# Kernel optimization log

Hardware: AMD Instinct MI355X
Metric: run time of the kernel (lower is better)

Reference implementation:

```python
import jax, jax.numpy as jnp
import numpy as np

N = 100000
E = 1600000
D_IN, D_HID, D_OUT = 128, 512, 256
EPS1 = 1e-9
BN_EPS = 1e-5


def setup_inputs() -> dict:
    key = jax.random.key(0)
    ks = jax.random.split(key, 8)
    return {
        "x": jax.random.normal(ks[0], (N, D_IN), dtype=jnp.float32),
        "edge_src": jax.random.randint(ks[1], (E,), 0, N, dtype=jnp.int32),
        "edge_dst": jax.random.randint(ks[2], (E,), 0, N, dtype=jnp.int32),
        "edge_weight": jax.random.uniform(ks[3], (E,), dtype=jnp.float32),
        "w1": jax.random.normal(ks[4], (D_IN, D_HID), dtype=jnp.float32) * (1.0 / np.sqrt(D_IN)),
        "b1": jnp.zeros((D_HID,), dtype=jnp.float32),
        "gamma": jnp.ones((D_HID,), dtype=jnp.float32),
        "beta": jnp.zeros((D_HID,), dtype=jnp.float32),
        "w2": jax.random.normal(ks[5], (D_HID, D_OUT), dtype=jnp.float32) * (1.0 / np.sqrt(D_HID)),
        "b2": jnp.zeros((D_OUT,), dtype=jnp.float32),
    }


def reference(x, edge_src, edge_dst, edge_weight, w1, b1, gamma, beta, w2, b2):
    # spmm(adj, x): gather source features, scale by edge weight, scatter-add to dst
    agg = jax.ops.segment_sum(x[edge_src] * edge_weight[:, None], edge_dst,
                              num_segments=x.shape[0])  # [N, D_IN]
    h = (1.0 + EPS1) * x + agg
    # mlp1: Linear -> BatchNorm1d (training-mode batch stats) -> ReLU -> Linear
    h = h @ w1 + b1  # [N, D_HID]
    mean = jnp.mean(h, axis=0)
    var = jnp.var(h, axis=0)  # biased variance, matching torch BN normalization
    h = (h - mean) * jax.lax.rsqrt(var + BN_EPS) * gamma + beta
    h = jax.nn.relu(h)
    return h @ w2 + b2  # [N, D_OUT]
```

## Files before the change

kernel.cpp:

```cpp
#include <hip/hip_runtime.h>
#include <hip/hip_bf16.h>

#define N_NODES 100000
#define N_EDGES 1600000
#define D_IN    128
#define D_HID   512
#define D_OUT   256

typedef __attribute__((ext_vector_type(8))) short bf16x8;
typedef __attribute__((ext_vector_type(4))) float f32x4;
typedef __attribute__((ext_vector_type(8))) unsigned short ushort8;

__device__ __forceinline__ short f2bf(float f) {
  union { float f; unsigned u; } un; un.f = f;
  unsigned r = un.u + 0x7fffu + ((un.u >> 16) & 1u);
  return (short)(r >> 16);
}
__device__ __forceinline__ float bf2f(unsigned short s) {
  union { unsigned u; float f; } un; un.u = ((unsigned)s) << 16; return un.f;
}
__device__ __forceinline__ void load_lds16(const void* g, void* l) {
  __builtin_amdgcn_global_load_lds(
      (const __attribute__((address_space(1))) char*)g,
      (__attribute__((address_space(3))) char*)l, 16, 0, 0);
}

__global__ __launch_bounds__(256) void k_prep(const float* __restrict__ w1,
                                              const float* __restrict__ w2,
                                              short* __restrict__ w1t,
                                              short* __restrict__ w2t,
                                              float* __restrict__ s1,
                                              float* __restrict__ s2,
                                              int* __restrict__ deg) {
  int gid = blockIdx.x * 256 + threadIdx.x;
  if (gid < D_IN * D_HID) {
    int n = gid >> 7, k = gid & 127;
    w1t[gid] = f2bf(w1[k * D_HID + n]);
  }
  int g2 = gid - D_IN * D_HID;
  if (g2 >= 0 && g2 < D_HID * D_OUT) {
    int n = g2 >> 9, k = g2 & 511;
    w2t[g2] = f2bf(w2[k * D_OUT + n]);
  }
  if (gid < D_HID) { s1[gid] = 0.f; s2[gid] = 0.f; }
  if (gid < N_NODES) deg[gid] = 0;
}

__global__ __launch_bounds__(256) void k_hist(const int* __restrict__ edst,
                                              int* __restrict__ deg) {
  int e = blockIdx.x * 256 + threadIdx.x;
  if (e < N_EDGES) atomicAdd(&deg[edst[e]], 1);
}

__global__ __launch_bounds__(1024) void k_scan(const int* __restrict__ deg,
                                               int* __restrict__ rowptr,
                                               int* __restrict__ cursor) {
  __shared__ int wsum[16];
  __shared__ int carry_s;
  int t = threadIdx.x;
  int lane = t & 63, w = t >> 6;
  if (t == 0) carry_s = 0;
  __syncthreads();
  for (int base = 0; base < N_NODES; base += 1024) {
    int i = base + t;
    int v = (i < N_NODES) ? deg[i] : 0;
    int sv = v;
    #pragma unroll
    for (int off = 1; off < 64; off <<= 1) {
      int u = __shfl_up(sv, off);
      if (lane >= off) sv += u;
    }
    if (lane == 63) wsum[w] = sv;
    __syncthreads();
    if (t < 16) {
      int ws = wsum[t];
      int ss = ws;
      #pragma unroll
      for (int off = 1; off < 16; off <<= 1) {
        int u = __shfl_up(ss, off);
        if (t >= off) ss += u;
      }
      wsum[t] = ss - ws;
    }
    __syncthreads();
    int incl = sv + wsum[w];
    int carry = carry_s;
    if (i < N_NODES) {
      int excl = carry + incl - v;
      rowptr[i] = excl;
      cursor[i] = excl;
    }
    __syncthreads();
    if (t == 1023) carry_s = carry + incl;
    __syncthreads();
  }
  if (t == 0) rowptr[N_NODES] = carry_s;
}

__global__ __launch_bounds__(256) void k_fill(const int* __restrict__ esrc,
                                              const int* __restrict__ edst,
                                              const float* __restrict__ ew,
                                              int* __restrict__ cursor,
                                              int2* __restrict__ recs) {
  int e = blockIdx.x * 256 + threadIdx.x;
  if (e < N_EDGES) {
    int d = edst[e];
    int slot = atomicAdd(&cursor[d], 1);
    int2 r;
    r.x = esrc[e];
    r.y = __float_as_int(ew[e]);
    recs[slot] = r;
  }
}

__global__ __launch_bounds__(256) void k_agg(const float* __restrict__ x,
                                             const int* __restrict__ rowptr,
                                             const int2* __restrict__ recs,
                                             unsigned short* __restrict__ aggb) {
  int gw = (blockIdx.x * 256 + threadIdx.x) >> 6;
  int lane = threadIdx.x & 63;
  if (gw >= N_NODES) return;
  int start = rowptr[gw], end = rowptr[gw + 1];
  float2 acc = *reinterpret_cast<const float2*>(x + (size_t)gw * D_IN + lane * 2);
  const float s0 = 1.0f + 1e-9f;
  acc.x *= s0; acc.y *= s0;
  for (int j = start; j < end; j += 64) {
    int cnt = end - j;
    if (cnt > 64) cnt = 64;
    int src = 0; float wt = 0.f;
    if (lane < cnt) {
      int2 r = recs[j + lane];
      src = r.x;
      wt = __int_as_float(r.y);
    }
    for (int jj = 0; jj < cnt; ++jj) {
      int s = __shfl(src, jj);
      float ww = __shfl(wt, jj);
      float2 xv = *reinterpret_cast<const float2*>(x + (size_t)s * D_IN + lane * 2);
      acc.x += ww * xv.x;
      acc.y += ww * xv.y;
    }
  }
  ushort2 o;
  o.x = (unsigned short)f2bf(acc.x);
  o.y = (unsigned short)f2bf(acc.y);
  *reinterpret_cast<ushort2*>(aggb + (size_t)gw * D_IN + lane * 2) = o;
}

__global__ __launch_bounds__(256) void k_gemm1(const unsigned short* __restrict__ aggb,
                                               const short* __restrict__ w1t,
                                               const float* __restrict__ b1,
                                               short* __restrict__ h1,
                                               float* __restrict__ s1,
                                               float* __restrict__ s2, int M) {
  __shared__ short As[128 * 64];
  __shared__ short Bs[128 * 64];
  int t = threadIdx.x;
  int bid = blockIdx.x;
  int nt = bid & 3, mt = bid >> 2;
  int wid = t >> 6, lane = t & 63;
  int wr = wid >> 1, wc = wid & 1;
  f32x4 acc[4][4] = {};

  for (int kt = 0; kt < 2; ++kt) {
    #pragma unroll
    for (int i = 0; i < 4; ++i) {
      int c = wid * 4 + i;
      int row = c * 8 + (lane >> 3);
      const unsigned short* g = aggb + (size_t)(mt * 128 + row) * D_IN + kt * 64 + (lane & 7) * 8;
      load_lds16(g, As + c * 512);
    }
    #pragma unroll
    for (int i = 0; i < 4; ++i) {
      int c = wid * 4 + i;
      int row = c * 8 + (lane >> 3);
      const short* g = w1t + (size_t)(nt * 128 + row) * D_IN + kt * 64 + (lane & 7) * 8;
      load_lds16(g, Bs + c * 512);
    }
    __syncthreads();
    #pragma unroll
    for (int kk = 0; kk < 2; ++kk) {
      bf16x8 af[4], bfr[4];
      #pragma unroll
      for (int mf = 0; mf < 4; ++mf)
        af[mf] = *reinterpret_cast<const bf16x8*>(As + (wr * 64 + mf * 16 + (lane & 15)) * 64 + kk * 32 + (lane >> 4) * 8);
      #pragma unroll
      for (int nf = 0; nf < 4; ++nf)
        bfr[nf] = *reinterpret_cast<const bf16x8*>(Bs + (wc * 64 + nf * 16 + (lane & 15)) * 64 + kk * 32 + (lane >> 4) * 8);
      #pragma unroll
      for (int mf = 0; mf < 4; ++mf)
        #pragma unroll
        for (int nf = 0; nf < 4; ++nf)
          acc[mf][nf] = __builtin_amdgcn_mfma_f32_16x16x32_bf16(af[mf], bfr[nf], acc[mf][nf], 0, 0, 0);
    }
    __syncthreads();
  }

  int colbase = nt * 128 + wc * 64;
  float ps[4] = {0, 0, 0, 0}, ps2[4] = {0, 0, 0, 0};
  #pragma unroll
  for (int mf = 0; mf < 4; ++mf)
    #pragma unroll
    for (int nf = 0; nf < 4; ++nf) {
      int col = colbase + nf * 16 + (lane & 15);
      float bb = b1[col];
      #pragma unroll
      for (int r = 0; r < 4; ++r) {
        int grow = mt * 128 + wr * 64 + mf * 16 + (lane >> 4) * 4 + r;
        if (grow < M) {
          float v = acc[mf][nf][r] + bb;
          h1[(size_t)grow * D_HID + col] = f2bf(v);
          ps[nf] += v; ps2[nf] += v * v;
        }
      }
    }
  #pragma unroll
  for (int nf = 0; nf < 4; ++nf) {
    float a = ps[nf], b = ps2[nf];
    a += __shfl_xor(a, 16); a += __shfl_xor(a, 32);
    b += __shfl_xor(b, 16); b += __shfl_xor(b, 32);
    if ((lane >> 4) == 0) {
      int col = colbase + nf * 16 + lane;
      unsafeAtomicAdd(&s1[col], a);
      unsafeAtomicAdd(&s2[col], b);
    }
  }
}

__global__ void k_bn(const float* __restrict__ s1, const float* __restrict__ s2,
                     const float* __restrict__ gamma, const float* __restrict__ beta,
                     float* __restrict__ A, float* __restrict__ C) {
  int i = threadIdx.x;
  float inv_n = 1.0f / (float)N_NODES;
  float mean = s1[i] * inv_n;
  float var = s2[i] * inv_n - mean * mean;
  float a = gamma[i] * rsqrtf(var + 1e-5f);
  A[i] = a;
  C[i] = beta[i] - mean * a;
}

__global__ __launch_bounds__(256) void k_gemm2(const unsigned short* __restrict__ h1,
                                               const short* __restrict__ w2t,
                                               const float* __restrict__ b2,
                                               const float* __restrict__ Abn,
                                               const float* __restrict__ Cbn,
                                               float* __restrict__ out, int M) {
  __shared__ short As[128 * 64];
  __shared__ short Bs[128 * 64];
  __shared__ float aL[D_HID], cL[D_HID];
  int t = threadIdx.x;
  for (int i = t; i < D_HID; i += 256) { aL[i] = Abn[i]; cL[i] = Cbn[i]; }
  __syncthreads();

  int bid = blockIdx.x;
  int nt = bid & 1, mt = bid >> 1;
  int wid = t >> 6, lane = t & 63;
  int wr = wid >> 1, wc = wid & 1;
  f32x4 acc[4][4] = {};

  for (int kt = 0; kt < 8; ++kt) {
    #pragma unroll
    for (int i = 0; i < 4; ++i) {
      int idx = i * 2048 + t * 8;
      int row = idx >> 6, k = idx & 63;
      int grow = mt * 128 + row;
      ushort8 res = {};
      if (grow < M) {
        ushort8 u = *reinterpret_cast<const ushort8*>(h1 + (size_t)grow * D_HID + kt * 64 + k);
        #pragma unroll
        for (int j = 0; j < 8; ++j) {
          int gk = kt * 64 + k + j;
          float v = bf2f(u[j]) * aL[gk] + cL[gk];
          v = fmaxf(v, 0.f);
          res[j] = (unsigned short)f2bf(v);
        }
      }
      *reinterpret_cast<ushort8*>(As + idx) = res;
    }
    #pragma unroll
    for (int i = 0; i < 4; ++i) {
      int c = wid * 4 + i;
      int row = c * 8 + (lane >> 3);
      const short* g = w2t + (size_t)(nt * 128 + row) * D_HID + kt * 64 + (lane & 7) * 8;
      load_lds16(g, Bs + c * 512);
    }
    __syncthreads();
    #pragma unroll
    for (int kk = 0; kk < 2; ++kk) {
      bf16x8 af[4], bfr[4];
      #pragma unroll
      for (int mf = 0; mf < 4; ++mf)
        af[mf] = *reinterpret_cast<const bf16x8*>(As + (wr * 64 + mf * 16 + (lane & 15)) * 64 + kk * 32 + (lane >> 4) * 8);
      #pragma unroll
      for (int nf = 0; nf < 4; ++nf)
        bfr[nf] = *reinterpret_cast<const bf16x8*>(Bs + (wc * 64 + nf * 16 + (lane & 15)) * 64 + kk * 32 + (lane >> 4) * 8);
      #pragma unroll
      for (int mf = 0; mf < 4; ++mf)
        #pragma unroll
        for (int nf = 0; nf < 4; ++nf)
          acc[mf][nf] = __builtin_amdgcn_mfma_f32_16x16x32_bf16(af[mf], bfr[nf], acc[mf][nf], 0, 0, 0);
    }
    __syncthreads();
  }

  int colbase = nt * 128 + wc * 64;
  #pragma unroll
  for (int mf = 0; mf < 4; ++mf)
    #pragma unroll
    for (int nf = 0; nf < 4; ++nf) {
      int col = colbase + nf * 16 + (lane & 15);
      float bb = b2[col];
      #pragma unroll
      for (int r = 0; r < 4; ++r) {
        int grow = mt * 128 + wr * 64 + mf * 16 + (lane >> 4) * 4 + r;
        if (grow < M) out[(size_t)grow * D_OUT + col] = acc[mf][nf][r] + bb;
      }
    }
}

extern "C" void kernel_launch(void* const* d_in, const int* in_sizes, int n_in,
                              void* d_out, int out_size, void* d_ws, size_t ws_size,
                              hipStream_t stream) {
  const float* x    = (const float*)d_in[0];
  const int* esrc   = (const int*)d_in[1];
  const int* edst   = (const int*)d_in[2];
  const float* ew   = (const float*)d_in[3];
  const float* w1   = (const float*)d_in[4];
  const float* b1   = (const float*)d_in[5];
  const float* gamma= (const float*)d_in[6];
  const float* beta = (const float*)d_in[7];
  const float* w2   = (const float*)d_in[8];
  const float* b2   = (const float*)d_in[9];
  float* out = (float*)d_out;

  char* base = (char*)d_ws;
  unsigned short* aggb = (unsigned short*)base;
  short* h1  = (short*)(base + 25600000);
  short* w1t = (short*)(base + 128000000);
  short* w2t = (short*)(base + 128131072);
  float* s1  = (float*)(base + 128393216);
  float* s2  = (float*)(base + 128395264);
  float* Abn = (float*)(base + 128397312);
  float* Cbn = (float*)(base + 128399360);
  int* rowptr = (int*)(base + 128401408);
  int* cursor = (int*)(base + 128801416);
  int* deg    = (int*)(base + 129201416);
  int2* recs  = (int2*)(base + 129601416);

  const int MT = (N_NODES + 127) / 128;

  k_prep<<<(D_IN * D_HID + D_HID * D_OUT + 255) / 256, 256, 0, stream>>>(w1, w2, w1t, w2t, s1, s2, deg);
  k_hist<<<(N_EDGES + 255) / 256, 256, 0, stream>>>(edst, deg);
  k_scan<<<1, 1024, 0, stream>>>(deg, rowptr, cursor);
  k_fill<<<(N_EDGES + 255) / 256, 256, 0, stream>>>(esrc, edst, ew, cursor, recs);
  k_agg<<<N_NODES * 64 / 256, 256, 0, stream>>>(x, rowptr, recs, aggb);
  k_gemm1<<<MT * 4, 256, 0, stream>>>(aggb, w1t, b1, h1, s1, s2, N_NODES);
  k_bn<<<1, D_HID, 0, stream>>>(s1, s2, gamma, beta, Abn, Cbn);
  k_gemm2<<<MT * 2, 256, 0, stream>>>((const unsigned short*)h1, w2t, b2, Abn, Cbn, out, N_NODES);
}
```

Measured before the change: 726.8 us.

## Parallelize CSR scan across blocks and gather bf16 features in aggregation

Replaces the single-block sequential prefix scan over node degrees with a three-kernel multi-block scan (per-block scan, block-sum scan, add-back). Adds a pre-pass converting x to bf16 into the h1 workspace region, so the edge-gather in aggregation reads half the bytes per neighbor. The bf16 conversion of x before accumulation adds rounding error relative to fp32 input, and it adds two extra kernel launches plus a full pass over x.

```diff
diff --git a/kernel.cpp b/kernel.cpp
--- a/kernel.cpp
+++ b/kernel.cpp
@@ -6,6 +6,7 @@
 #define D_IN    128
 #define D_HID   512
 #define D_OUT   256
+#define NB_SCAN ((N_NODES + 1023) / 1024)
 
 typedef __attribute__((ext_vector_type(8))) short bf16x8;
 typedef __attribute__((ext_vector_type(4))) float f32x4;
@@ -46,55 +47,83 @@
   if (gid < N_NODES) deg[gid] = 0;
 }
 
+__global__ __launch_bounds__(256) void k_xbf(const float* __restrict__ x,
+                                             short* __restrict__ xb) {
+  int gid = blockIdx.x * 256 + threadIdx.x;
+  const int total = N_NODES * D_IN / 4;
+  if (gid < total) {
+    float4 v = reinterpret_cast<const float4*>(x)[gid];
+    short4 o;
+    o.x = f2bf(v.x); o.y = f2bf(v.y); o.z = f2bf(v.z); o.w = f2bf(v.w);
+    reinterpret_cast<short4*>(xb)[gid] = o;
+  }
+}
+
 __global__ __launch_bounds__(256) void k_hist(const int* __restrict__ edst,
                                               int* __restrict__ deg) {
   int e = blockIdx.x * 256 + threadIdx.x;
   if (e < N_EDGES) atomicAdd(&deg[edst[e]], 1);
 }
 
-__global__ __launch_bounds__(1024) void k_scan(const int* __restrict__ deg,
-                                               int* __restrict__ rowptr,
-                                               int* __restrict__ cursor) {
+__global__ __launch_bounds__(1024) void k_scan1(const int* __restrict__ deg,
+                                                int* __restrict__ rowptr,
+                                                int* __restrict__ bsum) {
   __shared__ int wsum[16];
-  __shared__ int carry_s;
   int t = threadIdx.x;
   int lane = t & 63, w = t >> 6;
-  if (t == 0) carry_s = 0;
+  int i = blockIdx.x * 1024 + t;
+  int v = (i < N_NODES) ? deg[i] : 0;
+  int sv = v;
+  #pragma unroll
+  for (int off = 1; off < 64; off <<= 1) {
+    int u = __shfl_up(sv, off);
+    if (lane >= off) sv += u;
+  }
+  if (lane == 63) wsum[w] = sv;
   __syncthreads();
-  for (int base = 0; base < N_NODES; base += 1024) {
-    int i = base + t;
-    int v = (i < N_NODES) ? deg[i] : 0;
-    int sv = v;
-    #pragma unroll
-    for (int off = 1; off < 64; off <<= 1) {
-      int u = __shfl_up(sv, off);
-      if (lane >= off) sv += u;
-    }
-    if (lane == 63) wsum[w] = sv;
-    __syncthreads();
-    if (t < 16) {
-      int ws = wsum[t];
-      int ss = ws;
-      #pragma unroll
-      for (int off = 1; off < 16; off <<= 1) {
-        int u = __shfl_up(ss, off);
-        if (t >= off) ss += u;
-      }
-      wsum[t] = ss - ws;
-    }
-    __syncthreads();
-    int incl = sv + wsum[w];
-    int carry = carry_s;
-    if (i < N_NODES) {
-      int excl = carry + incl - v;
-      rowptr[i] = excl;
-      cursor[i] = excl;
-    }
-    __syncthreads();
-    if (t == 1023) carry_s = carry + incl;
-    __syncthreads();
-  }
-  if (t == 0) rowptr[N_NODES] = carry_s;
+  if (t < 16) {
+    int ws = wsum[t];
+    int ss = ws;
+    #pragma unroll
+    for (int off = 1; off < 16; off <<= 1) {
+      int u = __shfl_up(ss, off);
+      if (t >= off) ss += u;
+    }
+    wsum[t] = ss - ws;
+  }
+  __syncthreads();
+  int excl = sv - v + wsum[w];
+  if (i < N_NODES) rowptr[i] = excl;
+  if (t == 1023) bsum[blockIdx.x] = excl + v;
+}
+
+__global__ __launch_bounds__(64) void k_scan2(int* __restrict__ bsum,
+                                              int* __restrict__ rowptrN) {
+  int l = threadIdx.x;
+  int i0 = 2 * l, i1 = 2 * l + 1;
+  int v0 = (i0 < NB_SCAN) ? bsum[i0] : 0;
+  int v1 = (i1 < NB_SCAN) ? bsum[i1] : 0;
+  int p = v0 + v1, sv = p;
+  #pragma unroll
+  for (int off = 1; off < 64; off <<= 1) {
+    int u = __shfl_up(sv, off);
+    if (l >= off) sv += u;
+  }
+  int excl = sv - p;
+  if (i0 < NB_SCAN) bsum[i0] = excl;
+  if (i1 < NB_SCAN) bsum[i1] = excl + v0;
+  if (l == 63) *rowptrN = sv;
+}
+
+__global__ __launch_bounds__(256) void k_scan3(int* __restrict__ rowptr,
+                                               int* __restrict__ cursor,
+                                               const int* __restrict__ bsum) {
+  int i = blockIdx.x * 256 + threadIdx.x;
+  if (i < N_NODES) {
+    int v = rowptr[i] + bsum[i >> 10];
+    rowptr[i] = v;
+    cursor[i] = v;
+  }
 }
 
 __global__ __launch_bounds__(256) void k_fill(const int* __restrict__ esrc,
@@ -113,7 +142,7 @@
   }
 }
 
-__global__ __launch_bounds__(256) void k_agg(const float* __restrict__ x,
+__global__ __launch_bounds__(256) void k_agg(const unsigned short* __restrict__ xb,
                                              const int* __restrict__ rowptr,
                                              const int2* __restrict__ recs,
                                              unsigned short* __restrict__ aggb) {
@@ -121,9 +150,9 @@
   int lane = threadIdx.x & 63;
   if (gw >= N_NODES) return;
   int start = rowptr[gw], end = rowptr[gw + 1];
-  float2 acc = *reinterpret_cast<const float2*>(x + (size_t)gw * D_IN + lane * 2);
+  ushort2 sx = *reinterpret_cast<const ushort2*>(xb + (size_t)gw * D_IN + lane * 2);
   const float s0 = 1.0f + 1e-9f;
-  acc.x *= s0; acc.y *= s0;
+  float a0 = bf2f(sx.x) * s0, a1 = bf2f(sx.y) * s0;
   for (int j = start; j < end; j += 64) {
     int cnt = end - j;
     if (cnt > 64) cnt = 64;
@@ -136,14 +165,14 @@
     for (int jj = 0; jj < cnt; ++jj) {
       int s = __shfl(src, jj);
       float ww = __shfl(wt, jj);
-      float2 xv = *reinterpret_cast<const float2*>(x + (size_t)s * D_IN + lane * 2);
-      acc.x += ww * xv.x;
-      acc.y += ww * xv.y;
+      ushort2 xv = *reinterpret_cast<const ushort2*>(xb + (size_t)s * D_IN + lane * 2);
+      a0 += ww * bf2f(xv.x);
+      a1 += ww * bf2f(xv.y);
     }
   }
   ushort2 o;
-  o.x = (unsigned short)f2bf(acc.x);
-  o.y = (unsigned short)f2bf(acc.y);
+  o.x = (unsigned short)f2bf(a0);
+  o.y = (unsigned short)f2bf(a1);
   *reinterpret_cast<ushort2*>(aggb + (size_t)gw * D_IN + lane * 2) = o;
 }
 
@@ -336,6 +365,7 @@
   char* base = (char*)d_ws;
   unsigned short* aggb = (unsigned short*)base;
   short* h1  = (short*)(base + 25600000);
+  short* xbf = h1;
   short* w1t = (short*)(base + 128000000);
   short* w2t = (short*)(base + 128131072);
   float* s1  = (float*)(base + 128393216);
@@ -346,14 +376,18 @@
   int* cursor = (int*)(base + 128801416);
   int* deg    = (int*)(base + 129201416);
   int2* recs  = (int2*)(base + 129601416);
+  int* bsum   = (int*)(base + 142401416);
 
   const int MT = (N_NODES + 127) / 128;
 
   k_prep<<<(D_IN * D_HID + D_HID * D_OUT + 255) / 256, 256, 0, stream>>>(w1, w2, w1t, w2t, s1, s2, deg);
+  k_xbf<<<(N_NODES * D_IN / 4 + 255) / 256, 256, 0, stream>>>(x, xbf);
   k_hist<<<(N_EDGES + 255) / 256, 256, 0, stream>>>(edst, deg);
-  k_scan<<<1, 1024, 0, stream>>>(deg, rowptr, cursor);
+  k_scan1<<<NB_SCAN, 1024, 0, stream>>>(deg, rowptr, bsum);
+  k_scan2<<<1, 64, 0, stream>>>(bsum, rowptr + N_NODES);
+  k_scan3<<<(N_NODES + 255) / 256, 256, 0, stream>>>(rowptr, cursor, bsum);
   k_fill<<<(N_EDGES + 255) / 256, 256, 0, stream>>>(esrc, edst, ew, cursor, recs);
-  k_agg<<<N_NODES * 64 / 256, 256, 0, stream>>>(x, rowptr, recs, aggb);
+  k_agg<<<N_NODES * 64 / 256, 256, 0, stream>>>((const unsigned short*)xbf, rowptr, recs, aggb);
   k_gemm1<<<MT * 4, 256, 0, stream>>>(aggb, w1t, b1, h1, s1, s2, N_NODES);
   k_bn<<<1, D_HID, 0, stream>>>(s1, s2, gamma, beta, Abn, Cbn);
   k_gemm2<<<MT * 2, 256, 0, stream>>>((const unsigned short*)h1, w2t, b2, Abn, Cbn, out, N_NODES);
```

After: 629.1 us. 13.4% less time.

## Bucket edges into 64-node blocks and aggregate bf16 features via LDS atomics

Applied to the files above, without the earlier changes.

Replaces the per-node CSR build (node histogram, 100k-element single-block scan, per-node atomic fill) with a coarse bucketing scheme. Edges are grouped into 64-node buckets split across 8 groups, with LDS-privatized histograms and a small one-pass scan. The local destination index is packed into the high bits of the source index. Aggregation runs one block per bucket, gathers bf16-converted x and accumulates into an LDS float tile with shared-memory atomics. This cuts atomic contention and scan cost and halves gather bytes, but adds an extra conversion pass, LDS atomic traffic, and bf16 rounding of x before aggregation.

```diff
diff --git a/kernel.cpp b/kernel.cpp
--- a/kernel.cpp
+++ b/kernel.cpp
@@ -6,6 +6,12 @@
 #define D_IN    128
 #define D_HID   512
 #define D_OUT   256
+#define BKT     64
+#define NB      ((N_NODES + BKT - 1) / BKT)
+#define NGRP    8
+#define NCNT    (NB * NGRP)
+#define FB      512
+#define CH      ((N_EDGES + FB - 1) / FB)
 
 typedef __attribute__((ext_vector_type(8))) short bf16x8;
 typedef __attribute__((ext_vector_type(4))) float f32x4;
@@ -31,7 +37,7 @@
                                               short* __restrict__ w2t,
                                               float* __restrict__ s1,
                                               float* __restrict__ s2,
-                                              int* __restrict__ deg) {
+                                              int* __restrict__ hist) {
   int gid = blockIdx.x * 256 + threadIdx.x;
   if (gid < D_IN * D_HID) {
     int n = gid >> 7, k = gid & 127;
@@ -43,108 +49,140 @@
     w2t[g2] = f2bf(w2[k * D_OUT + n]);
   }
   if (gid < D_HID) { s1[gid] = 0.f; s2[gid] = 0.f; }
-  if (gid < N_NODES) deg[gid] = 0;
-}
-
-__global__ __launch_bounds__(256) void k_hist(const int* __restrict__ edst,
-                                              int* __restrict__ deg) {
-  int e = blockIdx.x * 256 + threadIdx.x;
-  if (e < N_EDGES) atomicAdd(&deg[edst[e]], 1);
-}
-
-__global__ __launch_bounds__(1024) void k_scan(const int* __restrict__ deg,
-                                               int* __restrict__ rowptr,
-                                               int* __restrict__ cursor) {
+  if (gid < NCNT) hist[gid] = 0;
+}
+
+__global__ __launch_bounds__(256) void k_xbf(const float* __restrict__ x,
+                                             short* __restrict__ xb) {
+  int gid = blockIdx.x * 256 + threadIdx.x;
+  const int total = N_NODES * D_IN / 4;
+  if (gid < total) {
+    float4 v = reinterpret_cast<const float4*>(x)[gid];
+    short4 o;
+    o.x = f2bf(v.x); o.y = f2bf(v.y); o.z = f2bf(v.z); o.w = f2bf(v.w);
+    reinterpret_cast<short4*>(xb)[gid] = o;
+  }
+}
+
+__global__ __launch_bounds__(256) void k_bhist(const int* __restrict__ edst,
+                                               int* __restrict__ hist) {
+  __shared__ int lh[NB];
+  int t = threadIdx.x, k = blockIdx.x, g = k & 7;
+  for (int i = t; i < NB; i += 256) lh[i] = 0;
+  __syncthreads();
+  int lim = min((k + 1) * CH, N_EDGES);
+  for (int e = k * CH + t; e < lim; e += 256)
+    atomicAdd(&lh[edst[e] >> 6], 1);
+  __syncthreads();
+  for (int i = t; i < NB; i += 256)
+    if (lh[i]) atomicAdd(&hist[i * NGRP + g], lh[i]);
+}
+
+__global__ __launch_bounds__(1024) void k_bscan(const int* __restrict__ hist,
+                                                int* __restrict__ rp2,
+                                                int* __restrict__ cur2) {
   __shared__ int wsum[16];
-  __shared__ int carry_s;
-  int t = threadIdx.x;
-  int lane = t & 63, w = t >> 6;
-  if (t == 0) carry_s = 0;
-  __syncthreads();
-  for (int base = 0; base < N_NODES; base += 1024) {
-    int i = base + t;
-    int v = (i < N_NODES) ? deg[i] : 0;
-    int sv = v;
-    #pragma unroll
-    for (int off = 1; off < 64; off <<= 1) {
-      int u = __shfl_up(sv, off);
-      if (lane >= off) sv += u;
-    }
-    if (lane == 63) wsum[w] = sv;
-    __syncthreads();
-    if (t < 16) {
-      int ws = wsum[t];
-      int ss = ws;
-      #pragma unroll
-      for (int off = 1; off < 16; off <<= 1) {
-        int u = __shfl_up(ss, off);
-        if (t >= off) ss += u;
-      }
-      wsum[t] = ss - ws;
-    }
-    __syncthreads();
-    int incl = sv + wsum[w];
-    int carry = carry_s;
-    if (i < N_NODES) {
-      int excl = carry + incl - v;
-      rowptr[i] = excl;
-      cursor[i] = excl;
-    }
-    __syncthreads();
-    if (t == 1023) carry_s = carry + incl;
-    __syncthreads();
-  }
-  if (t == 0) rowptr[N_NODES] = carry_s;
-}
-
-__global__ __launch_bounds__(256) void k_fill(const int* __restrict__ esrc,
-                                              const int* __restrict__ edst,
-                                              const float* __restrict__ ew,
-                                              int* __restrict__ cursor,
-                                              int2* __restrict__ recs) {
-  int e = blockIdx.x * 256 + threadIdx.x;
-  if (e < N_EDGES) {
+  int t = threadIdx.x, lane = t & 63, w = t >> 6;
+  int v[16];
+  int base = t * 16, tsum = 0;
+  #pragma unroll
+  for (int q = 0; q < 16; ++q) {
+    v[q] = (base + q < NCNT) ? hist[base + q] : 0;
+    tsum += v[q];
+  }
+  int sv = tsum;
+  #pragma unroll
+  for (int off = 1; off < 64; off <<= 1) {
+    int u = __shfl_up(sv, off);
+    if (lane >= off) sv += u;
+  }
+  if (lane == 63) wsum[w] = sv;
+  __syncthreads();
+  if (t < 16) {
+    int ws = wsum[t], ss = ws;
+    #pragma unroll
+    for (int off = 1; off < 16; off <<= 1) {
+      int u = __shfl_up(ss, off);
+      if (t >= off) ss += u;
+    }
+    wsum[t] = ss - ws;
+  }
+  __syncthreads();
+  int run = sv - tsum + wsum[w];
+  #pragma unroll
+  for (int q = 0; q < 16; ++q) {
+    if (base + q < NCNT) { rp2[base + q] = run; cur2[base + q] = run; }
+    run += v[q];
+  }
+  if (t == 1023) rp2[NCNT] = run;
+}
+
+__global__ __launch_bounds__(256) void k_bfill(const int* __restrict__ esrc,
+                                               const int* __restrict__ edst,
+                                               const float* __restrict__ ew,
+                                               int* __restrict__ cur2,
+                                               int2* __restrict__ recs) {
+  int t = threadIdx.x, k = blockIdx.x, g = k & 7;
+  int lim = min((k + 1) * CH, N_EDGES);
+  for (int e = k * CH + t; e < lim; e += 256) {
     int d = edst[e];
-    int slot = atomicAdd(&cursor[d], 1);
+    int slot = atomicAdd(&cur2[(d >> 6) * NGRP + g], 1);
     int2 r;
-    r.x = esrc[e];
+    r.x = esrc[e] | ((d & 63) << 20);
     r.y = __float_as_int(ew[e]);
     recs[slot] = r;
   }
 }
 
-__global__ __launch_bounds__(256) void k_agg(const float* __restrict__ x,
-                                             const int* __restrict__ rowptr,
-                                             const int2* __restrict__ recs,
-                                             unsigned short* __restrict__ aggb) {
-  int gw = (blockIdx.x * 256 + threadIdx.x) >> 6;
-  int lane = threadIdx.x & 63;
-  if (gw >= N_NODES) return;
-  int start = rowptr[gw], end = rowptr[gw + 1];
-  float2 acc = *reinterpret_cast<const float2*>(x + (size_t)gw * D_IN + lane * 2);
-  const float s0 = 1.0f + 1e-9f;
-  acc.x *= s0; acc.y *= s0;
-  for (int j = start; j < end; j += 64) {
-    int cnt = end - j;
+__global__ __launch_bounds__(256) void k_aggf(const unsigned short* __restrict__ xb,
+                                              const int* __restrict__ rp2,
+                                              const int2* __restrict__ recs,
+                                              unsigned short* __restrict__ aggb) {
+  __shared__ float accf[BKT * D_IN];
+  int t = threadIdx.x, b = blockIdx.x;
+  int lane = t & 63, wid = t >> 6;
+  #pragma unroll
+  for (int i = 0; i < 8; ++i)
+    *reinterpret_cast<f32x4*>(&accf[(i * 256 + t) * 4]) = f32x4{0.f, 0.f, 0.f, 0.f};
+  __syncthreads();
+  int s0 = rp2[b * NGRP], e0 = rp2[b * NGRP + NGRP];
+  for (int j = s0 + wid * 64; j < e0; j += 256) {
+    int cnt = e0 - j;
     if (cnt > 64) cnt = 64;
-    int src = 0; float wt = 0.f;
+    int pk = 0; float wt = 0.f;
     if (lane < cnt) {
       int2 r = recs[j + lane];
-      src = r.x;
+      pk = r.x;
       wt = __int_as_float(r.y);
     }
     for (int jj = 0; jj < cnt; ++jj) {
-      int s = __shfl(src, jj);
+      int p = __shfl(pk, jj);
       float ww = __shfl(wt, jj);
-      float2 xv = *reinterpret_cast<const float2*>(x + (size_t)s * D_IN + lane * 2);
-      acc.x += ww * xv.x;
-      acc.y += ww * xv.y;
-    }
-  }
-  ushort2 o;
-  o.x = (unsigned short)f2bf(acc.x);
-  o.y = (unsigned short)f2bf(acc.y);
-  *reinterpret_cast<ushort2*>(aggb + (size_t)gw * D_IN + lane * 2) = o;
+      int s = p & 0xFFFFF;
+      int ld = p >> 20;
+      ushort2 xv = *reinterpret_cast<const ushort2*>(xb + (size_t)s * D_IN + lane * 2);
+      atomicAdd(&accf[ld * D_IN + lane * 2], ww * bf2f(xv.x));
+      atomicAdd(&accf[ld * D_IN + lane * 2 + 1], ww * bf2f(xv.y));
+    }
+  }
+  __syncthreads();
+  const float s0c = 1.0f + 1e-9f;
+  #pragma unroll
+  for (int i = 0; i < 4; ++i) {
+    int idx = i * 256 + t;
+    int node = idx >> 4, c8 = (idx & 15) * 8;
+    int gnode = b * BKT + node;
+    if (gnode < N_NODES) {
+      ushort8 xr = *reinterpret_cast<const ushort8*>(xb + (size_t)gnode * D_IN + c8);
+      ushort8 o;
+      #pragma unroll
+      for (int q = 0; q < 8; ++q) {
+        float v = accf[node * D_IN + c8 + q] + s0c * bf2f(xr[q]);
+        o[q] = (unsigned short)f2bf(v);
+      }
+      *reinterpret_cast<ushort8*>(aggb + (size_t)gnode * D_IN + c8) = o;
+    }
+  }
 }
 
 __global__ __launch_bounds__(256) void k_gemm1(const unsigned short* __restrict__ aggb,
@@ -336,24 +374,26 @@
   char* base = (char*)d_ws;
   unsigned short* aggb = (unsigned short*)base;
   short* h1  = (short*)(base + 25600000);
+  short* xbf = h1;
   short* w1t = (short*)(base + 128000000);
   short* w2t = (short*)(base + 128131072);
   float* s1  = (float*)(base + 128393216);
   float* s2  = (float*)(base + 128395264);
   float* Abn = (float*)(base + 128397312);
   float* Cbn = (float*)(base + 128399360);
-  int* rowptr = (int*)(base + 128401408);
-  int* cursor = (int*)(base + 128801416);
-  int* deg    = (int*)(base + 129201416);
-  int2* recs  = (int2*)(base + 129601416);
+  int* rp2   = (int*)(base + 128401408);
+  int* cur2  = (int*)(base + 128451432);
+  int* hist  = (int*)(base + 128501456);
+  int2* recs = (int2*)(base + 129000000);
 
   const int MT = (N_NODES + 127) / 128;
 
-  k_prep<<<(D_IN * D_HID + D_HID * D_OUT + 255) / 256, 256, 0, stream>>>(w1, w2, w1t, w2t, s1, s2, deg);
-  k_hist<<<(N_EDGES + 255) / 256, 256, 0, stream>>>(edst, deg);
-  k_scan<<<1, 1024, 0, stream>>>(deg, rowptr, cursor);
-  k_fill<<<(N_EDGES + 255) / 256, 256, 0, stream>>>(esrc, edst, ew, cursor, recs);
-  k_agg<<<N_NODES * 64 / 256, 256, 0, stream>>>(x, rowptr, recs, aggb);
+  k_prep<<<(D_IN * D_HID + D_HID * D_OUT + 255) / 256, 256, 0, stream>>>(w1, w2, w1t, w2t, s1, s2, hist);
+  k_xbf<<<(N_NODES * D_IN / 4 + 255) / 256, 256, 0, stream>>>(x, xbf);
+  k_bhist<<<FB, 256, 0, stream>>>(edst, hist);
+  k_bscan<<<1, 1024, 0, stream>>>(hist, rp2, cur2);
+  k_bfill<<<FB, 256, 0, stream>>>(esrc, edst, ew, cur2, recs);
+  k_aggf<<<NB, 256, 0, stream>>>((const unsigned short*)xbf, rp2, recs, aggb);
   k_gemm1<<<MT * 4, 256, 0, stream>>>(aggb, w1t, b1, h1, s1, s2, N_NODES);
   k_bn<<<1, D_HID, 0, stream>>>(s1, s2, gamma, beta, Abn, Cbn);
   k_gemm2<<<MT * 2, 256, 0, stream>>>((const unsigned short*)h1, w2t, b2, Abn, Cbn, out, N_NODES);
```

Result: slower. 1.675 ms (+130.5%).
